# Kernel optimization log

Measured on AMD Instinct MI355X. Metric: run time of the kernel, lower is better.

## Reference

```python
import jax, jax.numpy as jnp
import numpy as np

EPS = 1e-5

def _layernorm(x, gamma, beta):
    # LayerNormalization over last axis (channels), epsilon=1e-5
    mu = jnp.mean(x, axis=-1, keepdims=True)
    var = jnp.var(x, axis=-1, keepdims=True)
    return (x - mu) * jax.lax.rsqrt(var + EPS) * gamma + beta

def setup_inputs() -> dict:
    key = jax.random.key(0)
    ks = jax.random.split(key, 6)
    B, H, W, C = 8, 64, 64, 256
    std = 0.1  # NIN init_scale
    return {
        "x": jax.random.normal(ks[0], (B, H, W, C), dtype=jnp.float32),
        "ln_gamma": jnp.ones((C,), dtype=jnp.float32),
        "ln_beta": jnp.zeros((C,), dtype=jnp.float32),
        "wq": jax.random.normal(ks[1], (C, C), dtype=jnp.float32) * std,
        "bq": jnp.zeros((C,), dtype=jnp.float32),
        "wk": jax.random.normal(ks[2], (C, C), dtype=jnp.float32) * std,
        "bk": jnp.zeros((C,), dtype=jnp.float32),
        "wv": jax.random.normal(ks[3], (C, C), dtype=jnp.float32) * std,
        "bv": jnp.zeros((C,), dtype=jnp.float32),
        "wo": jax.random.normal(ks[4], (C, C), dtype=jnp.float32) * std,
        "bo": jnp.zeros((C,), dtype=jnp.float32),
    }

def reference(x, ln_gamma, ln_beta, wq, bq, wk, bk, wv, bv, wo, bo):
    B, H, W, C = x.shape
    h = _layernorm(x, ln_gamma, ln_beta)
    # 1x1 convs == per-pixel channel matmuls
    q = jnp.einsum('bhwc,cd->bhwd', h, wq) + bq
    k = jnp.einsum('bhwc,cd->bhwd', h, wk) + bk
    v = jnp.einsum('bhwc,cd->bhwd', h, wv) + bv
    scale = jnp.float32(C) ** -0.5
    # dense spatial attention over all H*W tokens
    w = jnp.einsum('bhwc,bijc->bhwij', q, k) * scale  # [B,H,W,H,W]
    w = jax.nn.softmax(w.reshape(B, H, W, H * W), axis=-1).reshape(B, H, W, H, W)
    h = jnp.einsum('bhwij,bijc->bhwc', w, v)
    h = jnp.einsum('bhwc,cd->bhwd', h, wo) + bo
    return x + h
```

## Files before the change

### kernel.cpp

```cpp
#include <hip/hip_runtime.h>
#include <stdint.h>

#define NB    8
#define NTOK  4096
#define TOK   32768
#define CDIM  256
#define BQ    128
#define BK    64
#define NT    (NTOK / BK)

#define KPITCH 264
#define VPITCH 68
#define KTILE_SH (BK * KPITCH)
#define VTILE_SH (CDIM * VPITCH)
#define KCH   33
#define VCH   34
#define TOTCH (KCH + VCH)

typedef __attribute__((ext_vector_type(8))) short bf16x8;
typedef __attribute__((ext_vector_type(4))) float f32x4;

#define SSCALE 0.09016844f

static __device__ __forceinline__ unsigned short f2bf(float f) {
    union { float f; unsigned u; } v; v.f = f;
    unsigned r = v.u + 0x7fffu + ((v.u >> 16) & 1u);
    return (unsigned short)(r >> 16);
}

static __device__ __forceinline__ void dma16(const unsigned short* g, unsigned short* l) {
    __builtin_amdgcn_global_load_lds(
        (const __attribute__((address_space(1))) unsigned int*)g,
        (__attribute__((address_space(3))) unsigned int*)l,
        16, 0, 0);
}

__global__ __launch_bounds__(256) void prep_kernel(
        const float* __restrict__ x,
        const float* __restrict__ gamma,
        const float* __restrict__ beta,
        const float* __restrict__ w0, const float* __restrict__ w1,
        const float* __restrict__ w2, const float* __restrict__ w3,
        unsigned short* __restrict__ h_bf,
        unsigned short* __restrict__ wt) {
    int bx = blockIdx.x;
    if (bx >= TOK / 4) {
        int id = bx - TOK / 4;
        int m = id >> 8, dd = id & 255;
        const float* src = (m == 0) ? w0 : (m == 1) ? w1 : (m == 2) ? w2 : w3;
        wt[m * (CDIM * CDIM) + dd * CDIM + threadIdx.x] = f2bf(src[threadIdx.x * CDIM + dd]);
        return;
    }
    int w = threadIdx.x >> 6;
    int lane = threadIdx.x & 63;
    int token = bx * 4 + w;
    const float4 xv = ((const float4*)(x + (size_t)token * CDIM))[lane];
    float s = xv.x + xv.y + xv.z + xv.w;
    #pragma unroll
    for (int off = 1; off < 64; off <<= 1) s += __shfl_xor(s, off, 64);
    float mean = s * (1.0f / 256.0f);
    float d0 = xv.x - mean, d1 = xv.y - mean, d2 = xv.z - mean, d3 = xv.w - mean;
    float ss = d0 * d0 + d1 * d1 + d2 * d2 + d3 * d3;
    #pragma unroll
    for (int off = 1; off < 64; off <<= 1) ss += __shfl_xor(ss, off, 64);
    float rstd = rsqrtf(ss * (1.0f / 256.0f) + 1e-5f);
    float4 g = ((const float4*)gamma)[lane];
    float4 b = ((const float4*)beta)[lane];
    ushort4 o;
    o.x = f2bf(d0 * rstd * g.x + b.x);
    o.y = f2bf(d1 * rstd * g.y + b.y);
    o.z = f2bf(d2 * rstd * g.z + b.z);
    o.w = f2bf(d3 * rstd * g.w + b.w);
    ((ushort4*)(h_bf + (size_t)token * CDIM))[lane] = o;
}

__global__ __launch_bounds__(128) void qkv_kernel(
        const unsigned short* __restrict__ h_bf,
        const unsigned short* __restrict__ wts,
        const float* __restrict__ bq,
        const float* __restrict__ bk,
        const float* __restrict__ bv,
        unsigned short* __restrict__ q_bf,
        unsigned short* __restrict__ k2,
        unsigned short* __restrict__ vt2) {
    __shared__ unsigned short VT[64][VPITCH];
    int tid = threadIdx.x;
    int w = tid >> 6, lane = tid & 63, quad = lane >> 4, l16 = lane & 15;
    int blk = blockIdx.x;
    int gy = blockIdx.y;
    int nt0 = gy * 4;
    int tok_base = blk * 64 + w * 32;

    bf16x8 afr[2][8];
    #pragma unroll
    for (int s = 0; s < 2; ++s)
        #pragma unroll
        for (int kk = 0; kk < 8; ++kk)
            afr[s][kk] = *(const bf16x8*)(h_bf + (size_t)(tok_base + s * 16 + l16) * CDIM + kk * 32 + quad * 8);

    {
        const unsigned short* wq_t = wts;
        #pragma unroll
        for (int ntl = 0; ntl < 4; ++ntl) {
            int nt = nt0 + ntl;
            f32x4 acc0 = {0.f, 0.f, 0.f, 0.f};
            f32x4 acc1 = {0.f, 0.f, 0.f, 0.f};
            #pragma unroll
            for (int kk = 0; kk < 8; ++kk) {
                bf16x8 bfr = *(const bf16x8*)(wq_t + (size_t)(nt * 16 + l16) * CDIM + kk * 32 + quad * 8);
                acc0 = __builtin_amdgcn_mfma_f32_16x16x32_bf16(afr[0][kk], bfr, acc0, 0, 0, 0);
                acc1 = __builtin_amdgcn_mfma_f32_16x16x32_bf16(afr[1][kk], bfr, acc1, 0, 0, 0);
            }
            int d = nt * 16 + l16;
            float bb = bq[d];
            #pragma unroll
            for (int r = 0; r < 4; ++r) {
                q_bf[(size_t)(tok_base + quad * 4 + r) * CDIM + d]      = f2bf((acc0[r] + bb) * SSCALE);
                q_bf[(size_t)(tok_base + 16 + quad * 4 + r) * CDIM + d] = f2bf((acc1[r] + bb) * SSCALE);
            }
        }
    }
    {
        const unsigned short* wk_t = wts + CDIM * CDIM;
        unsigned short* kdst = k2 + (size_t)blk * KTILE_SH;
        int row0 = w * 32 + quad * 4;
        #pragma unroll
        for (int ntl = 0; ntl < 4; ++ntl) {
            int nt = nt0 + ntl;
            f32x4 acc0 = {0.f, 0.f, 0.f, 0.f};
            f32x4 acc1 = {0.f, 0.f, 0.f, 0.f};
            #pragma unroll
            for (int kk = 0; kk < 8; ++kk) {
                bf16x8 bfr = *(const bf16x8*)(wk_t + (size_t)(nt * 16 + l16) * CDIM + kk * 32 + quad * 8);
                acc0 = __builtin_amdgcn_mfma_f32_16x16x32_bf16(afr[0][kk], bfr, acc0, 0, 0, 0);
                acc1 = __builtin_amdgcn_mfma_f32_16x16x32_bf16(afr[1][kk], bfr, acc1, 0, 0, 0);
            }
            int d = nt * 16 + l16;
            float bb = bk[d];
            #pragma unroll
            for (int r = 0; r < 4; ++r) {
                kdst[(size_t)(row0 + r) * KPITCH + d]      = f2bf(acc0[r] + bb);
                kdst[(size_t)(row0 + 16 + r) * KPITCH + d] = f2bf(acc1[r] + bb);
            }
        }
    }
    {
        const unsigned short* wv_t = wts + 2 * CDIM * CDIM;
        int col0 = w * 32 + quad * 4;
        #pragma unroll
        for (int ntl = 0; ntl < 4; ++ntl) {
            int nt = nt0 + ntl;
            f32x4 acc0 = {0.f, 0.f, 0.f, 0.f};
            f32x4 acc1 = {0.f, 0.f, 0.f, 0.f};
            #pragma unroll
            for (int kk = 0; kk < 8; ++kk) {
                bf16x8 bfr = *(const bf16x8*)(wv_t + (size_t)(nt * 16 + l16) * CDIM + kk * 32 + quad * 8);
                acc0 = __builtin_amdgcn_mfma_f32_16x16x32_bf16(afr[0][kk], bfr, acc0, 0, 0, 0);
                acc1 = __builtin_amdgcn_mfma_f32_16x16x32_bf16(afr[1][kk], bfr, acc1, 0, 0, 0);
            }
            int d = nt * 16 + l16;
            float bb = bv[d];
            int dl = ntl * 16 + l16;
            #pragma unroll
            for (int r = 0; r < 4; ++r) {
                VT[dl][col0 + r]      = f2bf(acc0[r] + bb);
                VT[dl][col0 + 16 + r] = f2bf(acc1[r] + bb);
            }
        }
    }
    __syncthreads();
    const uint4* src = (const uint4*)(&VT[0][0]);
    uint4* dst = (uint4*)(vt2 + (size_t)blk * VTILE_SH + (size_t)gy * 64 * VPITCH);
    #pragma unroll
    for (int i = 0; i < 4; ++i)
        dst[i * 128 + tid] = src[i * 128 + tid];
    if (tid < 32) dst[512 + tid] = src[512 + tid];
}

#define DMA_TILE(KS, VS, ktn)                                                        \
    {                                                                                \
        const unsigned short* gk = k2 + (size_t)(b * NT + (ktn)) * KTILE_SH;         \
        const unsigned short* gv = vt2 + (size_t)(b * NT + (ktn)) * VTILE_SH;        \
        for (int c = w; c < TOTCH; c += 8) {                                         \
            if (c < KCH) dma16(gk + c * 512 + lane * 8, &KS[0][0] + c * 512);        \
            else dma16(gv + (c - KCH) * 512 + lane * 8, &VS[0][0] + (c - KCH) * 512);\
        }                                                                            \
    }

#define COMPUTE_TILE(KS, VS)                                                         \
    {                                                                                \
        f32x4 sfr[2][2];                                                             \
        _Pragma("unroll")                                                            \
        for (int nt = 0; nt < 2; ++nt) {                                             \
            f32x4 a0 = {0.f, 0.f, 0.f, 0.f};                                         \
            f32x4 a1 = {0.f, 0.f, 0.f, 0.f};                                         \
            _Pragma("unroll")                                                        \
            for (int kk = 0; kk < 8; ++kk) {                                         \
                bf16x8 kb = *(const bf16x8*)(&KS[kh * 32 + nt * 16 + l16][kk * 32 + quad * 8]); \
                a0 = __builtin_amdgcn_mfma_f32_16x16x32_bf16(qfr[0][kk], kb, a0, 0, 0, 0);      \
                a1 = __builtin_amdgcn_mfma_f32_16x16x32_bf16(qfr[1][kk], kb, a1, 0, 0, 0);      \
            }                                                                        \
            sfr[0][nt] = a0; sfr[1][nt] = a1;                                        \
        }                                                                            \
        _Pragma("unroll")                                                            \
        for (int s = 0; s < 2; ++s)                                                  \
            _Pragma("unroll")                                                        \
            for (int nt = 0; nt < 2; ++nt)                                           \
                _Pragma("unroll")                                                    \
                for (int r = 0; r < 4; ++r) {                                        \
                    float p = exp2f(sfr[s][nt][r]);                                  \
                    lacc[s][r] += p;                                                 \
                    Pl[wq * 32 + s * 16 + quad * 4 + r][kh * 32 + nt * 16 + l16] =   \
                        (unsigned short)(__float_as_uint(p) >> 16);                  \
                }                                                                    \
        bf16x8 pfr0 = *(const bf16x8*)(&Pl[wq * 32 + l16][kh * 32 + quad * 8]);      \
        bf16x8 pfr1 = *(const bf16x8*)(&Pl[wq * 32 + 16 + l16][kh * 32 + quad * 8]); \
        _Pragma("unroll")                                                            \
        for (int nt2 = 0; nt2 < 16; ++nt2) {                                         \
            bf16x8 vb = *(const bf16x8*)(&VS[nt2 * 16 + l16][kh * 32 + quad * 8]);   \
            O[0][nt2] = __builtin_amdgcn_mfma_f32_16x16x32_bf16(pfr0, vb, O[0][nt2], 0, 0, 0);  \
            O[1][nt2] = __builtin_amdgcn_mfma_f32_16x16x32_bf16(pfr1, vb, O[1][nt2], 0, 0, 0);  \
        }                                                                            \
    }

__global__ __launch_bounds__(512, 2) void flash_kernel(
        const unsigned short* __restrict__ q_bf,
        const unsigned short* __restrict__ k2,
        const unsigned short* __restrict__ vt2,
        unsigned short* __restrict__ attn) {
    __shared__ unsigned short Ks0[BK][KPITCH];
    __shared__ unsigned short Ks1[BK][KPITCH];
    __shared__ unsigned short Vs0[CDIM][VPITCH];
    __shared__ unsigned short Vs1[CDIM][VPITCH];
    __shared__ unsigned short Pl[BQ][VPITCH];

    int tid = threadIdx.x;
    int w = tid >> 6, lane = tid & 63, quad = lane >> 4, l16 = lane & 15;
    int kh = w >> 2;
    int wq = w & 3;
    int bid = blockIdx.x;
    int b = bid & 7;
    int qtile = bid >> 3;
    int qrow = qtile * BQ + wq * 32;
    const size_t bbase = (size_t)b * NTOK * CDIM;

    bf16x8 qfr[2][8];
    #pragma unroll
    for (int s = 0; s < 2; ++s)
        #pragma unroll
        for (int kk = 0; kk < 8; ++kk)
            qfr[s][kk] = *(const bf16x8*)(q_bf + bbase + (size_t)(qrow + s * 16 + l16) * CDIM + kk * 32 + quad * 8);

    f32x4 O[2][16];
    #pragma unroll
    for (int s = 0; s < 2; ++s)
        #pragma unroll
        for (int i = 0; i < 16; ++i) O[s][i] = (f32x4){0.f, 0.f, 0.f, 0.f};
    float lacc[2][4] = {{0.f, 0.f, 0.f, 0.f}, {0.f, 0.f, 0.f, 0.f}};

    DMA_TILE(Ks0, Vs0, 0);
    __syncthreads();

    for (int kt2 = 0; kt2 < NT; kt2 += 2) {
        DMA_TILE(Ks1, Vs1, kt2 + 1);
        COMPUTE_TILE(Ks0, Vs0);
        __syncthreads();
        if (kt2 + 2 < NT) DMA_TILE(Ks0, Vs0, kt2 + 2);
        COMPUTE_TILE(Ks1, Vs1);
        __syncthreads();
    }

    float* sO = (wq == 0) ? (float*)&Ks0[0][0] : (wq == 1) ? (float*)&Ks1[0][0]
              : (wq == 2) ? (float*)&Vs0[0][0] : (float*)&Vs1[0][0];
    float* sL = (float*)&Pl[0][0] + wq * 512;

    if (kh == 1) {
        #pragma unroll
        for (int s = 0; s < 2; ++s) {
            #pragma unroll
            for (int nt2 = 0; nt2 < 16; ++nt2)
                #pragma unroll
                for (int r = 0; r < 4; ++r)
                    sO[((s * 16 + nt2) * 4 + r) * 64 + lane] = O[s][nt2][r];
            #pragma unroll
            for (int r = 0; r < 4; ++r)
                sL[(s * 4 + r) * 64 + lane] = lacc[s][r];
        }
    }
    __syncthreads();
    if (kh == 0) {
        float linv[2][4];
        #pragma unroll
        for (int s = 0; s < 2; ++s)
            #pragma unroll
            for (int r = 0; r < 4; ++r) {
                float ls = lacc[s][r] + sL[(s * 4 + r) * 64 + lane];
                #pragma unroll
                for (int off = 1; off < 16; off <<= 1)
                    ls += __shfl_xor(ls, off, 64);
                linv[s][r] = 1.0f / ls;
            }
        #pragma unroll
        for (int s = 0; s < 2; ++s)
            #pragma unroll
            for (int nt2 = 0; nt2 < 16; ++nt2) {
                int d = nt2 * 16 + l16;
                #pragma unroll
                for (int r = 0; r < 4; ++r) {
                    float val = (O[s][nt2][r] + sO[((s * 16 + nt2) * 4 + r) * 64 + lane]) * linv[s][r];
                    attn[bbase + (size_t)(qrow + s * 16 + quad * 4 + r) * CDIM + d] = f2bf(val);
                }
            }
    }
}

__global__ __launch_bounds__(128) void oproj_kernel(
        const unsigned short* __restrict__ attn,
        const unsigned short* __restrict__ wo_t,
        const float* __restrict__ bo,
        const float* __restrict__ x,
        float* __restrict__ out) {
    int w = threadIdx.x >> 6, lane = threadIdx.x & 63;
    int quad = lane >> 4, l16 = lane & 15;
    int tok_base = blockIdx.x * 64 + w * 32;
    int nt0 = blockIdx.y * 8;

    bf16x8 afr[2][8];
    #pragma unroll
    for (int s = 0; s < 2; ++s)
        #pragma unroll
        for (int kk = 0; kk < 8; ++kk)
            afr[s][kk] = *(const bf16x8*)(attn + (size_t)(tok_base + s * 16 + l16) * CDIM + kk * 32 + quad * 8);

    #pragma unroll
    for (int ntl = 0; ntl < 8; ++ntl) {
        int nt = nt0 + ntl;
        f32x4 acc0 = {0.f, 0.f, 0.f, 0.f};
        f32x4 acc1 = {0.f, 0.f, 0.f, 0.f};
        #pragma unroll
        for (int kk = 0; kk < 8; ++kk) {
            bf16x8 bfr = *(const bf16x8*)(wo_t + (size_t)(nt * 16 + l16) * CDIM + kk * 32 + quad * 8);
            acc0 = __builtin_amdgcn_mfma_f32_16x16x32_bf16(afr[0][kk], bfr, acc0, 0, 0, 0);
            acc1 = __builtin_amdgcn_mfma_f32_16x16x32_bf16(afr[1][kk], bfr, acc1, 0, 0, 0);
        }
        int d = nt * 16 + l16;
        float bb = bo[d];
        #pragma unroll
        for (int r = 0; r < 4; ++r) {
            size_t idx0 = (size_t)(tok_base + quad * 4 + r) * CDIM + d;
            size_t idx1 = (size_t)(tok_base + 16 + quad * 4 + r) * CDIM + d;
            out[idx0] = x[idx0] + acc0[r] + bb;
            out[idx1] = x[idx1] + acc1[r] + bb;
        }
    }
}

extern "C" void kernel_launch(void* const* d_in, const int* in_sizes, int n_in,
                              void* d_out, int out_size, void* d_ws, size_t ws_size,
                              hipStream_t stream) {
    const float* x     = (const float*)d_in[0];
    const float* gamma = (const float*)d_in[1];
    const float* beta  = (const float*)d_in[2];
    const float* wq    = (const float*)d_in[3];
    const float* bq    = (const float*)d_in[4];
    const float* wk    = (const float*)d_in[5];
    const float* bk    = (const float*)d_in[6];
    const float* wv    = (const float*)d_in[7];
    const float* bv    = (const float*)d_in[8];
    const float* wo    = (const float*)d_in[9];
    const float* bo    = (const float*)d_in[10];
    float* out = (float*)d_out;

    char* ws = (char*)d_ws;
    unsigned short* h_bf = (unsigned short*)(ws);
    unsigned short* q_bf = (unsigned short*)(ws + 16777216);
    unsigned short* k2   = (unsigned short*)(ws + 33554432);
    unsigned short* vt2  = (unsigned short*)(ws + 50855936);
    unsigned short* wt   = (unsigned short*)(ws + 68681728);
    unsigned short* attn = h_bf;

    prep_kernel<<<TOK / 4 + 1024, 256, 0, stream>>>(x, gamma, beta, wq, wk, wv, wo, h_bf, wt);
    qkv_kernel<<<dim3(TOK / 64, 4), 128, 0, stream>>>(h_bf, wt, bq, bk, bv, q_bf, k2, vt2);
    flash_kernel<<<(NTOK / BQ) * NB, 512, 0, stream>>>(q_bf, k2, vt2, attn);
    oproj_kernel<<<dim3(TOK / 64, 2), 128, 0, stream>>>(attn, wt + 3 * (CDIM * CDIM), bo, x, out);
}
```

Baseline: 362.3 us.

## Split attention KV range across blocks and merge partials in separate combine kernel

```diff
diff --git a/kernel.cpp b/kernel.cpp
--- a/kernel.cpp
+++ b/kernel.cpp
@@ -5,17 +5,20 @@
 #define NTOK  4096
 #define TOK   32768
 #define CDIM  256
-#define BQ    128
-#define BK    64
-#define NT    (NTOK / BK)
-
-#define KPITCH 264
-#define VPITCH 68
-#define KTILE_SH (BK * KPITCH)
-#define VTILE_SH (CDIM * VPITCH)
-#define KCH   33
-#define VCH   34
-#define TOTCH (KCH + VCH)
+
+#define BQ2   128
+#define BK2   32
+#define NTB   128
+#define NT2   64
+
+#define KP2   272
+#define VP2   32
+#define PLP   36
+#define KTILE2_SH (BK2 * KP2)
+#define VTILE2_SH (CDIM * VP2)
+#define KCH2  17
+#define VCH2  16
+#define TOTCH2 (KCH2 + VCH2)
 
 typedef __attribute__((ext_vector_type(8))) short bf16x8;
 typedef __attribute__((ext_vector_type(4))) float f32x4;
@@ -83,7 +86,7 @@
         unsigned short* __restrict__ q_bf,
         unsigned short* __restrict__ k2,
         unsigned short* __restrict__ vt2) {
-    __shared__ unsigned short VT[64][VPITCH];
+    __shared__ unsigned short VT[64][72];
     int tid = threadIdx.x;
     int w = tid >> 6, lane = tid & 63, quad = lane >> 4, l16 = lane & 15;
     int blk = blockIdx.x;
@@ -122,8 +125,7 @@
     }
     {
         const unsigned short* wk_t = wts + CDIM * CDIM;
-        unsigned short* kdst = k2 + (size_t)blk * KTILE_SH;
-        int row0 = w * 32 + quad * 4;
+        unsigned short* kdst = k2 + (size_t)(blk * 2 + w) * KTILE2_SH;
         #pragma unroll
         for (int ntl = 0; ntl < 4; ++ntl) {
             int nt = nt0 + ntl;
@@ -139,8 +141,8 @@
             float bb = bk[d];
             #pragma unroll
             for (int r = 0; r < 4; ++r) {
-                kdst[(size_t)(row0 + r) * KPITCH + d]      = f2bf(acc0[r] + bb);
-                kdst[(size_t)(row0 + 16 + r) * KPITCH + d] = f2bf(acc1[r] + bb);
+                kdst[(size_t)(quad * 4 + r) * KP2 + d]      = f2bf(acc0[r] + bb);
+                kdst[(size_t)(quad * 4 + 16 + r) * KP2 + d] = f2bf(acc1[r] + bb);
             }
         }
     }
@@ -169,87 +171,102 @@
         }
     }
     __syncthreads();
-    const uint4* src = (const uint4*)(&VT[0][0]);
-    uint4* dst = (uint4*)(vt2 + (size_t)blk * VTILE_SH + (size_t)gy * 64 * VPITCH);
-    #pragma unroll
-    for (int i = 0; i < 4; ++i)
-        dst[i * 128 + tid] = src[i * 128 + tid];
-    if (tid < 32) dst[512 + tid] = src[512 + tid];
-}
-
-#define DMA_TILE(KS, VS, ktn)                                                        \
+    #pragma unroll
+    for (int j = 0; j < 4; ++j) {
+        int idx = j * 128 + tid;
+        int half = idx >> 8;
+        int rem = idx & 255;
+        int rr = rem >> 2;
+        int c4 = rem & 3;
+        const uint4* src = (const uint4*)(&VT[rr][half * 32 + c4 * 8]);
+        uint4* dst = (uint4*)(vt2 + (size_t)(blk * 2 + half) * VTILE2_SH
+                                   + (size_t)(gy * 64 + rr) * VP2 + c4 * 8);
+        *dst = *src;
+    }
+}
+
+#define DMA2(KS, VS, tl)                                                             \
     {                                                                                \
-        const unsigned short* gk = k2 + (size_t)(b * NT + (ktn)) * KTILE_SH;         \
-        const unsigned short* gv = vt2 + (size_t)(b * NT + (ktn)) * VTILE_SH;        \
-        for (int c = w; c < TOTCH; c += 8) {                                         \
-            if (c < KCH) dma16(gk + c * 512 + lane * 8, &KS[0][0] + c * 512);        \
-            else dma16(gv + (c - KCH) * 512 + lane * 8, &VS[0][0] + (c - KCH) * 512);\
+        const unsigned short* gk = k2 + (size_t)(tg0 + (tl)) * KTILE2_SH;            \
+        const unsigned short* gv = vt2 + (size_t)(tg0 + (tl)) * VTILE2_SH;           \
+        _Pragma("unroll")                                                            \
+        for (int i = 0; i < 9; ++i) {                                                \
+            int c = w + i * 4;                                                       \
+            if (c < TOTCH2) {                                                        \
+                if (c < KCH2) dma16(gk + c * 512 + lane * 8, &KS[0][0] + c * 512);   \
+                else dma16(gv + (c - KCH2) * 512 + lane * 8, &VS[0][0] + (c - KCH2) * 512); \
+            }                                                                        \
         }                                                                            \
     }
 
-#define COMPUTE_TILE(KS, VS)                                                         \
+#define COMPUTE2(KS, VS)                                                             \
     {                                                                                \
         f32x4 sfr[2][2];                                                             \
+        __builtin_amdgcn_s_setprio(1);                                               \
         _Pragma("unroll")                                                            \
         for (int nt = 0; nt < 2; ++nt) {                                             \
             f32x4 a0 = {0.f, 0.f, 0.f, 0.f};                                         \
             f32x4 a1 = {0.f, 0.f, 0.f, 0.f};                                         \
             _Pragma("unroll")                                                        \
             for (int kk = 0; kk < 8; ++kk) {                                         \
-                bf16x8 kb = *(const bf16x8*)(&KS[kh * 32 + nt * 16 + l16][kk * 32 + quad * 8]); \
-                a0 = __builtin_amdgcn_mfma_f32_16x16x32_bf16(qfr[0][kk], kb, a0, 0, 0, 0);      \
-                a1 = __builtin_amdgcn_mfma_f32_16x16x32_bf16(qfr[1][kk], kb, a1, 0, 0, 0);      \
+                bf16x8 kb = *(const bf16x8*)(&KS[nt * 16 + l16][kk * 32 + quad * 8]); \
+                a0 = __builtin_amdgcn_mfma_f32_16x16x32_bf16(qfr[0][kk], kb, a0, 0, 0, 0); \
+                a1 = __builtin_amdgcn_mfma_f32_16x16x32_bf16(qfr[1][kk], kb, a1, 0, 0, 0); \
             }                                                                        \
             sfr[0][nt] = a0; sfr[1][nt] = a1;                                        \
         }                                                                            \
+        __builtin_amdgcn_s_setprio(0);                                               \
         _Pragma("unroll")                                                            \
         for (int s = 0; s < 2; ++s)                                                  \
             _Pragma("unroll")                                                        \
             for (int nt = 0; nt < 2; ++nt)                                           \
                 _Pragma("unroll")                                                    \
                 for (int r = 0; r < 4; ++r) {                                        \
-                    float p = exp2f(sfr[s][nt][r]);                                  \
+                    float p = __builtin_amdgcn_exp2f(sfr[s][nt][r]);                 \
                     lacc[s][r] += p;                                                 \
-                    Pl[wq * 32 + s * 16 + quad * 4 + r][kh * 32 + nt * 16 + l16] =   \
-                        (unsigned short)(__float_as_uint(p) >> 16);                  \
+                    Pl[w * 32 + s * 16 + quad * 4 + r][nt * 16 + l16] = f2bf(p);     \
                 }                                                                    \
-        bf16x8 pfr0 = *(const bf16x8*)(&Pl[wq * 32 + l16][kh * 32 + quad * 8]);      \
-        bf16x8 pfr1 = *(const bf16x8*)(&Pl[wq * 32 + 16 + l16][kh * 32 + quad * 8]); \
+        bf16x8 pfr0 = *(const bf16x8*)(&Pl[w * 32 + l16][quad * 8]);                 \
+        bf16x8 pfr1 = *(const bf16x8*)(&Pl[w * 32 + 16 + l16][quad * 8]);            \
+        __builtin_amdgcn_s_setprio(1);                                               \
         _Pragma("unroll")                                                            \
         for (int nt2 = 0; nt2 < 16; ++nt2) {                                         \
-            bf16x8 vb = *(const bf16x8*)(&VS[nt2 * 16 + l16][kh * 32 + quad * 8]);   \
-            O[0][nt2] = __builtin_amdgcn_mfma_f32_16x16x32_bf16(pfr0, vb, O[0][nt2], 0, 0, 0);  \
-            O[1][nt2] = __builtin_amdgcn_mfma_f32_16x16x32_bf16(pfr1, vb, O[1][nt2], 0, 0, 0);  \
+            bf16x8 vb = *(const bf16x8*)(&VS[nt2 * 16 + l16][quad * 8]);             \
+            O[0][nt2] = __builtin_amdgcn_mfma_f32_16x16x32_bf16(pfr0, vb, O[0][nt2], 0, 0, 0); \
+            O[1][nt2] = __builtin_amdgcn_mfma_f32_16x16x32_bf16(pfr1, vb, O[1][nt2], 0, 0, 0); \
         }                                                                            \
-    }
-
-__global__ __launch_bounds__(512, 2) void flash_kernel(
+        __builtin_amdgcn_s_setprio(0);                                               \
+    }
+
+__global__ __launch_bounds__(256, 2) void flash_kernel(
         const unsigned short* __restrict__ q_bf,
         const unsigned short* __restrict__ k2,
         const unsigned short* __restrict__ vt2,
-        unsigned short* __restrict__ attn) {
-    __shared__ unsigned short Ks0[BK][KPITCH];
-    __shared__ unsigned short Ks1[BK][KPITCH];
-    __shared__ unsigned short Vs0[CDIM][VPITCH];
-    __shared__ unsigned short Vs1[CDIM][VPITCH];
-    __shared__ unsigned short Pl[BQ][VPITCH];
+        unsigned short* __restrict__ attn1,
+        float* __restrict__ attn0,
+        float* __restrict__ lws) {
+    __shared__ unsigned short Ks0[BK2][KP2];
+    __shared__ unsigned short Ks1[BK2][KP2];
+    __shared__ unsigned short Vs0[CDIM][VP2];
+    __shared__ unsigned short Vs1[CDIM][VP2];
+    __shared__ unsigned short Pl[BQ2][PLP];
 
     int tid = threadIdx.x;
     int w = tid >> 6, lane = tid & 63, quad = lane >> 4, l16 = lane & 15;
-    int kh = w >> 2;
-    int wq = w & 3;
     int bid = blockIdx.x;
     int b = bid & 7;
-    int qtile = bid >> 3;
-    int qrow = qtile * BQ + wq * 32;
-    const size_t bbase = (size_t)b * NTOK * CDIM;
+    int qtile = (bid >> 3) & 31;
+    int kh2 = bid >> 8;
+    int qrow = qtile * BQ2 + w * 32;
+    int rowb = b * NTOK + qrow;
+    int tg0 = b * NTB + kh2 * NT2;
 
     bf16x8 qfr[2][8];
     #pragma unroll
     for (int s = 0; s < 2; ++s)
         #pragma unroll
         for (int kk = 0; kk < 8; ++kk)
-            qfr[s][kk] = *(const bf16x8*)(q_bf + bbase + (size_t)(qrow + s * 16 + l16) * CDIM + kk * 32 + quad * 8);
+            qfr[s][kk] = *(const bf16x8*)(q_bf + (size_t)(rowb + s * 16 + l16) * CDIM + kk * 32 + quad * 8);
 
     f32x4 O[2][16];
     #pragma unroll
@@ -258,60 +275,83 @@
         for (int i = 0; i < 16; ++i) O[s][i] = (f32x4){0.f, 0.f, 0.f, 0.f};
     float lacc[2][4] = {{0.f, 0.f, 0.f, 0.f}, {0.f, 0.f, 0.f, 0.f}};
 
-    DMA_TILE(Ks0, Vs0, 0);
+    DMA2(Ks0, Vs0, 0);
     __syncthreads();
 
-    for (int kt2 = 0; kt2 < NT; kt2 += 2) {
-        DMA_TILE(Ks1, Vs1, kt2 + 1);
-        COMPUTE_TILE(Ks0, Vs0);
+    for (int kt2 = 0; kt2 < NT2; kt2 += 2) {
+        DMA2(Ks1, Vs1, kt2 + 1);
+        COMPUTE2(Ks0, Vs0);
         __syncthreads();
-        if (kt2 + 2 < NT) DMA_TILE(Ks0, Vs0, kt2 + 2);
-        COMPUTE_TILE(Ks1, Vs1);
+        if (kt2 + 2 < NT2) DMA2(Ks0, Vs0, kt2 + 2);
+        COMPUTE2(Ks1, Vs1);
         __syncthreads();
     }
 
-    float* sO = (wq == 0) ? (float*)&Ks0[0][0] : (wq == 1) ? (float*)&Ks1[0][0]
-              : (wq == 2) ? (float*)&Vs0[0][0] : (float*)&Vs1[0][0];
-    float* sL = (float*)&Pl[0][0] + wq * 512;
-
-    if (kh == 1) {
-        #pragma unroll
-        for (int s = 0; s < 2; ++s) {
+    float lred[2][4];
+    #pragma unroll
+    for (int s = 0; s < 2; ++s)
+        #pragma unroll
+        for (int r = 0; r < 4; ++r) {
+            float ls = lacc[s][r];
+            #pragma unroll
+            for (int off = 1; off < 16; off <<= 1) ls += __shfl_xor(ls, off, 64);
+            lred[s][r] = ls;
+        }
+    if (l16 == 0) {
+        #pragma unroll
+        for (int s = 0; s < 2; ++s)
+            #pragma unroll
+            for (int r = 0; r < 4; ++r)
+                lws[kh2 * TOK + rowb + s * 16 + quad * 4 + r] = lred[s][r];
+    }
+    if (kh2 == 0) {
+        #pragma unroll
+        for (int s = 0; s < 2; ++s)
             #pragma unroll
             for (int nt2 = 0; nt2 < 16; ++nt2)
                 #pragma unroll
                 for (int r = 0; r < 4; ++r)
-                    sO[((s * 16 + nt2) * 4 + r) * 64 + lane] = O[s][nt2][r];
-            #pragma unroll
-            for (int r = 0; r < 4; ++r)
-                sL[(s * 4 + r) * 64 + lane] = lacc[s][r];
-        }
-    }
-    __syncthreads();
-    if (kh == 0) {
-        float linv[2][4];
+                    attn0[(size_t)(rowb + s * 16 + quad * 4 + r) * CDIM + nt2 * 16 + l16] = O[s][nt2][r];
+    } else {
         #pragma unroll
         for (int s = 0; s < 2; ++s)
             #pragma unroll
-            for (int r = 0; r < 4; ++r) {
-                float ls = lacc[s][r] + sL[(s * 4 + r) * 64 + lane];
+            for (int nt2 = 0; nt2 < 16; ++nt2)
                 #pragma unroll
-                for (int off = 1; off < 16; off <<= 1)
-                    ls += __shfl_xor(ls, off, 64);
-                linv[s][r] = 1.0f / ls;
-            }
-        #pragma unroll
-        for (int s = 0; s < 2; ++s)
-            #pragma unroll
-            for (int nt2 = 0; nt2 < 16; ++nt2) {
-                int d = nt2 * 16 + l16;
-                #pragma unroll
-                for (int r = 0; r < 4; ++r) {
-                    float val = (O[s][nt2][r] + sO[((s * 16 + nt2) * 4 + r) * 64 + lane]) * linv[s][r];
-                    attn[bbase + (size_t)(qrow + s * 16 + quad * 4 + r) * CDIM + d] = f2bf(val);
-                }
-            }
-    }
+                for (int r = 0; r < 4; ++r)
+                    attn1[(size_t)(rowb + s * 16 + quad * 4 + r) * CDIM + nt2 * 16 + l16] = f2bf(O[s][nt2][r]);
+    }
+}
+
+__global__ __launch_bounds__(256) void combine_kernel(
+        const float* __restrict__ p0,
+        unsigned short* __restrict__ p1,
+        const float* __restrict__ lws) {
+    int t = blockIdx.x * 256 + threadIdx.x;
+    int row = t >> 5;
+    int c8 = (t & 31) * 8;
+    float inv = 1.0f / (lws[row] + lws[TOK + row]);
+    const float4* a = (const float4*)(p0 + (size_t)row * CDIM + c8);
+    float4 x0 = a[0], x1 = a[1];
+    uint4 bv = *(const uint4*)(p1 + (size_t)row * CDIM + c8);
+    float f0 = __uint_as_float((bv.x & 0xffffu) << 16);
+    float f1 = __uint_as_float(bv.x & 0xffff0000u);
+    float f2 = __uint_as_float((bv.y & 0xffffu) << 16);
+    float f3 = __uint_as_float(bv.y & 0xffff0000u);
+    float f4 = __uint_as_float((bv.z & 0xffffu) << 16);
+    float f5 = __uint_as_float(bv.z & 0xffff0000u);
+    float f6 = __uint_as_float((bv.w & 0xffffu) << 16);
+    float f7 = __uint_as_float(bv.w & 0xffff0000u);
+    float v0 = (x0.x + f0) * inv, v1 = (x0.y + f1) * inv;
+    float v2 = (x0.z + f2) * inv, v3 = (x0.w + f3) * inv;
+    float v4 = (x1.x + f4) * inv, v5 = (x1.y + f5) * inv;
+    float v6 = (x1.z + f6) * inv, v7 = (x1.w + f7) * inv;
+    uint4 o;
+    o.x = (unsigned)f2bf(v0) | ((unsigned)f2bf(v1) << 16);
+    o.y = (unsigned)f2bf(v2) | ((unsigned)f2bf(v3) << 16);
+    o.z = (unsigned)f2bf(v4) | ((unsigned)f2bf(v5) << 16);
+    o.w = (unsigned)f2bf(v6) | ((unsigned)f2bf(v7) << 16);
+    *(uint4*)(p1 + (size_t)row * CDIM + c8) = o;
 }
 
 __global__ __launch_bounds__(128) void oproj_kernel(
@@ -375,12 +415,14 @@
     unsigned short* h_bf = (unsigned short*)(ws);
     unsigned short* q_bf = (unsigned short*)(ws + 16777216);
     unsigned short* k2   = (unsigned short*)(ws + 33554432);
-    unsigned short* vt2  = (unsigned short*)(ws + 50855936);
-    unsigned short* wt   = (unsigned short*)(ws + 68681728);
+    unsigned short* vt2  = (unsigned short*)(ws + 51380224);
+    unsigned short* wt   = (unsigned short*)(ws + 68157440);
+    float* lws           = (float*)(ws + 68681728);
     unsigned short* attn = h_bf;
 
     prep_kernel<<<TOK / 4 + 1024, 256, 0, stream>>>(x, gamma, beta, wq, wk, wv, wo, h_bf, wt);
     qkv_kernel<<<dim3(TOK / 64, 4), 128, 0, stream>>>(h_bf, wt, bq, bk, bv, q_bf, k2, vt2);
-    flash_kernel<<<(NTOK / BQ) * NB, 512, 0, stream>>>(q_bf, k2, vt2, attn);
+    flash_kernel<<<512, 256, 0, stream>>>(q_bf, k2, vt2, attn, out, lws);
+    combine_kernel<<<TOK * 32 / 256, 256, 0, stream>>>(out, attn, lws);
     oproj_kernel<<<dim3(TOK / 64, 2), 128, 0, stream>>>(attn, wt + 3 * (CDIM * CDIM), bo, x, out);
 }
```

New measurement: 410.4 us. 1.13x slower.

## Swizzle K/V tiles instead of padding, use vmcnt-based pipelining and setprio

Applied to the files above, without the earlier changes.

```diff
diff --git a/kernel.cpp b/kernel.cpp
--- a/kernel.cpp
+++ b/kernel.cpp
@@ -9,13 +9,9 @@
 #define BK    64
 #define NT    (NTOK / BK)
 
-#define KPITCH 264
-#define VPITCH 68
-#define KTILE_SH (BK * KPITCH)
-#define VTILE_SH (CDIM * VPITCH)
-#define KCH   33
-#define VCH   34
-#define TOTCH (KCH + VCH)
+#define KTILE_SH (BK * CDIM)
+#define VTILE_SH (CDIM * BK)
+#define PLP   72
 
 typedef __attribute__((ext_vector_type(8))) short bf16x8;
 typedef __attribute__((ext_vector_type(4))) float f32x4;
@@ -83,7 +79,7 @@
         unsigned short* __restrict__ q_bf,
         unsigned short* __restrict__ k2,
         unsigned short* __restrict__ vt2) {
-    __shared__ unsigned short VT[64][VPITCH];
+    __shared__ unsigned short VT[64][PLP];
     int tid = threadIdx.x;
     int w = tid >> 6, lane = tid & 63, quad = lane >> 4, l16 = lane & 15;
     int blk = blockIdx.x;
@@ -139,8 +135,10 @@
             float bb = bk[d];
             #pragma unroll
             for (int r = 0; r < 4; ++r) {
-                kdst[(size_t)(row0 + r) * KPITCH + d]      = f2bf(acc0[r] + bb);
-                kdst[(size_t)(row0 + 16 + r) * KPITCH + d] = f2bf(acc1[r] + bb);
+                int k0 = row0 + r;
+                int ds = d ^ ((k0 & 7) << 3);
+                kdst[(size_t)k0 * 256 + ds]        = f2bf(acc0[r] + bb);
+                kdst[(size_t)(k0 + 16) * 256 + ds] = f2bf(acc1[r] + bb);
             }
         }
     }
@@ -169,58 +167,82 @@
         }
     }
     __syncthreads();
-    const uint4* src = (const uint4*)(&VT[0][0]);
-    uint4* dst = (uint4*)(vt2 + (size_t)blk * VTILE_SH + (size_t)gy * 64 * VPITCH);
-    #pragma unroll
-    for (int i = 0; i < 4; ++i)
-        dst[i * 128 + tid] = src[i * 128 + tid];
-    if (tid < 32) dst[512 + tid] = src[512 + tid];
+    #pragma unroll
+    for (int j = 0; j < 4; ++j) {
+        int idx = j * 128 + tid;
+        int rr = idx >> 3;
+        int c8 = idx & 7;
+        const uint4* src = (const uint4*)(&VT[rr][c8 * 8]);
+        int dsh = (gy * 64 + rr) * 64 + ((c8 * 8) ^ ((rr & 7) << 3));
+        *(uint4*)(vt2 + (size_t)blk * VTILE_SH + dsh) = *src;
+    }
 }
 
 #define DMA_TILE(KS, VS, ktn)                                                        \
     {                                                                                \
         const unsigned short* gk = k2 + (size_t)(b * NT + (ktn)) * KTILE_SH;         \
         const unsigned short* gv = vt2 + (size_t)(b * NT + (ktn)) * VTILE_SH;        \
-        for (int c = w; c < TOTCH; c += 8) {                                         \
-            if (c < KCH) dma16(gk + c * 512 + lane * 8, &KS[0][0] + c * 512);        \
-            else dma16(gv + (c - KCH) * 512 + lane * 8, &VS[0][0] + (c - KCH) * 512);\
+        _Pragma("unroll")                                                            \
+        for (int i = 0; i < 8; ++i) {                                                \
+            int c = w * 8 + i;                                                       \
+            if (c < 32) dma16(gk + c * 512 + lane * 8, &KS[0][0] + c * 512);         \
+            else dma16(gv + (c - 32) * 512 + lane * 8, &VS[0][0] + (c - 32) * 512);  \
         }                                                                            \
     }
+
+#define WAITV(N)                                             \
+    asm volatile("s_waitcnt vmcnt(" #N ")" ::: "memory");    \
+    __builtin_amdgcn_sched_barrier(0);                       \
+    __builtin_amdgcn_s_barrier();                            \
+    __builtin_amdgcn_sched_barrier(0);
+
+#define BARRIER()                                            \
+    __builtin_amdgcn_sched_barrier(0);                       \
+    __builtin_amdgcn_s_barrier();                            \
+    __builtin_amdgcn_sched_barrier(0);
 
 #define COMPUTE_TILE(KS, VS)                                                         \
     {                                                                                \
         f32x4 sfr[2][2];                                                             \
+        __builtin_amdgcn_s_setprio(1);                                               \
         _Pragma("unroll")                                                            \
         for (int nt = 0; nt < 2; ++nt) {                                             \
             f32x4 a0 = {0.f, 0.f, 0.f, 0.f};                                         \
             f32x4 a1 = {0.f, 0.f, 0.f, 0.f};                                         \
             _Pragma("unroll")                                                        \
             for (int kk = 0; kk < 8; ++kk) {                                         \
-                bf16x8 kb = *(const bf16x8*)(&KS[kh * 32 + nt * 16 + l16][kk * 32 + quad * 8]); \
+                bf16x8 kb = *(const bf16x8*)(&KS[0][0]                               \
+                    + (size_t)(kh * 32 + nt * 16 + l16) * 256                        \
+                    + ((kk * 32 + quad * 8) ^ swz));                                 \
                 a0 = __builtin_amdgcn_mfma_f32_16x16x32_bf16(qfr[0][kk], kb, a0, 0, 0, 0);      \
                 a1 = __builtin_amdgcn_mfma_f32_16x16x32_bf16(qfr[1][kk], kb, a1, 0, 0, 0);      \
             }                                                                        \
             sfr[0][nt] = a0; sfr[1][nt] = a1;                                        \
         }                                                                            \
+        __builtin_amdgcn_s_setprio(0);                                               \
         _Pragma("unroll")                                                            \
         for (int s = 0; s < 2; ++s)                                                  \
             _Pragma("unroll")                                                        \
             for (int nt = 0; nt < 2; ++nt)                                           \
                 _Pragma("unroll")                                                    \
                 for (int r = 0; r < 4; ++r) {                                        \
-                    float p = exp2f(sfr[s][nt][r]);                                  \
+                    float p = __builtin_amdgcn_exp2f(sfr[s][nt][r]);                 \
                     lacc[s][r] += p;                                                 \
                     Pl[wq * 32 + s * 16 + quad * 4 + r][kh * 32 + nt * 16 + l16] =   \
                         (unsigned short)(__float_as_uint(p) >> 16);                  \
                 }                                                                    \
         bf16x8 pfr0 = *(const bf16x8*)(&Pl[wq * 32 + l16][kh * 32 + quad * 8]);      \
         bf16x8 pfr1 = *(const bf16x8*)(&Pl[wq * 32 + 16 + l16][kh * 32 + quad * 8]); \
+        __builtin_amdgcn_s_setprio(1);                                               \
         _Pragma("unroll")                                                            \
         for (int nt2 = 0; nt2 < 16; ++nt2) {                                         \
-            bf16x8 vb = *(const bf16x8*)(&VS[nt2 * 16 + l16][kh * 32 + quad * 8]);   \
+            bf16x8 vb = *(const bf16x8*)(&VS[0][0]                                   \
+                + (size_t)(nt2 * 16 + l16) * 64                                      \
+                + ((kh * 32 + quad * 8) ^ swz));                                     \
             O[0][nt2] = __builtin_amdgcn_mfma_f32_16x16x32_bf16(pfr0, vb, O[0][nt2], 0, 0, 0);  \
             O[1][nt2] = __builtin_amdgcn_mfma_f32_16x16x32_bf16(pfr1, vb, O[1][nt2], 0, 0, 0);  \
         }                                                                            \
+        __builtin_amdgcn_s_setprio(0);                                               \
     }
 
 __global__ __launch_bounds__(512, 2) void flash_kernel(
@@ -228,16 +250,17 @@
         const unsigned short* __restrict__ k2,
         const unsigned short* __restrict__ vt2,
         unsigned short* __restrict__ attn) {
-    __shared__ unsigned short Ks0[BK][KPITCH];
-    __shared__ unsigned short Ks1[BK][KPITCH];
-    __shared__ unsigned short Vs0[CDIM][VPITCH];
-    __shared__ unsigned short Vs1[CDIM][VPITCH];
-    __shared__ unsigned short Pl[BQ][VPITCH];
+    __shared__ unsigned short Ks0[BK][256];
+    __shared__ unsigned short Ks1[BK][256];
+    __shared__ unsigned short Vs0[CDIM][64];
+    __shared__ unsigned short Vs1[CDIM][64];
+    __shared__ unsigned short Pl[BQ][PLP];
 
     int tid = threadIdx.x;
     int w = tid >> 6, lane = tid & 63, quad = lane >> 4, l16 = lane & 15;
     int kh = w >> 2;
     int wq = w & 3;
+    int swz = (l16 & 7) << 3;
     int bid = blockIdx.x;
     int b = bid & 7;
     int qtile = bid >> 3;
@@ -259,15 +282,20 @@
     float lacc[2][4] = {{0.f, 0.f, 0.f, 0.f}, {0.f, 0.f, 0.f, 0.f}};
 
     DMA_TILE(Ks0, Vs0, 0);
-    __syncthreads();
 
     for (int kt2 = 0; kt2 < NT; kt2 += 2) {
         DMA_TILE(Ks1, Vs1, kt2 + 1);
+        WAITV(8)
         COMPUTE_TILE(Ks0, Vs0);
-        __syncthreads();
-        if (kt2 + 2 < NT) DMA_TILE(Ks0, Vs0, kt2 + 2);
+        BARRIER()
+        if (kt2 + 2 < NT) {
+            DMA_TILE(Ks0, Vs0, kt2 + 2);
+            WAITV(8)
+        } else {
+            WAITV(0)
+        }
         COMPUTE_TILE(Ks1, Vs1);
-        __syncthreads();
+        BARRIER()
     }
 
     float* sO = (wq == 0) ? (float*)&Ks0[0][0] : (wq == 1) ? (float*)&Ks1[0][0]
@@ -375,8 +403,8 @@
     unsigned short* h_bf = (unsigned short*)(ws);
     unsigned short* q_bf = (unsigned short*)(ws + 16777216);
     unsigned short* k2   = (unsigned short*)(ws + 33554432);
-    unsigned short* vt2  = (unsigned short*)(ws + 50855936);
-    unsigned short* wt   = (unsigned short*)(ws + 68681728);
+    unsigned short* vt2  = (unsigned short*)(ws + 50331648);
+    unsigned short* wt   = (unsigned short*)(ws + 67108864);
     unsigned short* attn = h_bf;
 
     prep_kernel<<<TOK / 4 + 1024, 256, 0, stream>>>(x, gamma, beta, wq, wk, wv, wo, h_bf, wt);
```

New measurement: 502.0 us. 1.39x slower.

## Split flash attention block across 16 waves with 16 query rows each

Applied to the files above, without the earlier changes.

```diff
diff --git a/kernel.cpp b/kernel.cpp
--- a/kernel.cpp
+++ b/kernel.cpp
@@ -181,7 +181,7 @@
     {                                                                                \
         const unsigned short* gk = k2 + (size_t)(b * NT + (ktn)) * KTILE_SH;         \
         const unsigned short* gv = vt2 + (size_t)(b * NT + (ktn)) * VTILE_SH;        \
-        for (int c = w; c < TOTCH; c += 8) {                                         \
+        for (int c = w; c < TOTCH; c += 16) {                                        \
             if (c < KCH) dma16(gk + c * 512 + lane * 8, &KS[0][0] + c * 512);        \
             else dma16(gv + (c - KCH) * 512 + lane * 8, &VS[0][0] + (c - KCH) * 512);\
         }                                                                            \
@@ -189,41 +189,35 @@
 
 #define COMPUTE_TILE(KS, VS)                                                         \
     {                                                                                \
-        f32x4 sfr[2][2];                                                             \
+        f32x4 sfr[2];                                                                \
         _Pragma("unroll")                                                            \
         for (int nt = 0; nt < 2; ++nt) {                                             \
             f32x4 a0 = {0.f, 0.f, 0.f, 0.f};                                         \
-            f32x4 a1 = {0.f, 0.f, 0.f, 0.f};                                         \
             _Pragma("unroll")                                                        \
             for (int kk = 0; kk < 8; ++kk) {                                         \
                 bf16x8 kb = *(const bf16x8*)(&KS[kh * 32 + nt * 16 + l16][kk * 32 + quad * 8]); \
-                a0 = __builtin_amdgcn_mfma_f32_16x16x32_bf16(qfr[0][kk], kb, a0, 0, 0, 0);      \
-                a1 = __builtin_amdgcn_mfma_f32_16x16x32_bf16(qfr[1][kk], kb, a1, 0, 0, 0);      \
+                a0 = __builtin_amdgcn_mfma_f32_16x16x32_bf16(qfr[kk], kb, a0, 0, 0, 0);         \
             }                                                                        \
-            sfr[0][nt] = a0; sfr[1][nt] = a1;                                        \
+            sfr[nt] = a0;                                                            \
         }                                                                            \
         _Pragma("unroll")                                                            \
-        for (int s = 0; s < 2; ++s)                                                  \
+        for (int nt = 0; nt < 2; ++nt)                                               \
             _Pragma("unroll")                                                        \
-            for (int nt = 0; nt < 2; ++nt)                                           \
-                _Pragma("unroll")                                                    \
-                for (int r = 0; r < 4; ++r) {                                        \
-                    float p = exp2f(sfr[s][nt][r]);                                  \
-                    lacc[s][r] += p;                                                 \
-                    Pl[wq * 32 + s * 16 + quad * 4 + r][kh * 32 + nt * 16 + l16] =   \
-                        (unsigned short)(__float_as_uint(p) >> 16);                  \
-                }                                                                    \
-        bf16x8 pfr0 = *(const bf16x8*)(&Pl[wq * 32 + l16][kh * 32 + quad * 8]);      \
-        bf16x8 pfr1 = *(const bf16x8*)(&Pl[wq * 32 + 16 + l16][kh * 32 + quad * 8]); \
+            for (int r = 0; r < 4; ++r) {                                            \
+                float p = exp2f(sfr[nt][r]);                                         \
+                lacc[r] += p;                                                        \
+                Pl[wq * 16 + quad * 4 + r][kh * 32 + nt * 16 + l16] =                \
+                    (unsigned short)(__float_as_uint(p) >> 16);                      \
+            }                                                                        \
+        bf16x8 pfr = *(const bf16x8*)(&Pl[wq * 16 + l16][kh * 32 + quad * 8]);       \
         _Pragma("unroll")                                                            \
         for (int nt2 = 0; nt2 < 16; ++nt2) {                                         \
             bf16x8 vb = *(const bf16x8*)(&VS[nt2 * 16 + l16][kh * 32 + quad * 8]);   \
-            O[0][nt2] = __builtin_amdgcn_mfma_f32_16x16x32_bf16(pfr0, vb, O[0][nt2], 0, 0, 0);  \
-            O[1][nt2] = __builtin_amdgcn_mfma_f32_16x16x32_bf16(pfr1, vb, O[1][nt2], 0, 0, 0);  \
+            O[nt2] = __builtin_amdgcn_mfma_f32_16x16x32_bf16(pfr, vb, O[nt2], 0, 0, 0);         \
         }                                                                            \
     }
 
-__global__ __launch_bounds__(512, 2) void flash_kernel(
+__global__ __launch_bounds__(1024, 4) void flash_kernel(
         const unsigned short* __restrict__ q_bf,
         const unsigned short* __restrict__ k2,
         const unsigned short* __restrict__ vt2,
@@ -236,27 +230,23 @@
 
     int tid = threadIdx.x;
     int w = tid >> 6, lane = tid & 63, quad = lane >> 4, l16 = lane & 15;
-    int kh = w >> 2;
-    int wq = w & 3;
+    int kh = w >> 3;
+    int wq = w & 7;
     int bid = blockIdx.x;
     int b = bid & 7;
     int qtile = bid >> 3;
-    int qrow = qtile * BQ + wq * 32;
+    int qrow = qtile * BQ + wq * 16;
     const size_t bbase = (size_t)b * NTOK * CDIM;
 
-    bf16x8 qfr[2][8];
-    #pragma unroll
-    for (int s = 0; s < 2; ++s)
-        #pragma unroll
-        for (int kk = 0; kk < 8; ++kk)
-            qfr[s][kk] = *(const bf16x8*)(q_bf + bbase + (size_t)(qrow + s * 16 + l16) * CDIM + kk * 32 + quad * 8);
-
-    f32x4 O[2][16];
-    #pragma unroll
-    for (int s = 0; s < 2; ++s)
-        #pragma unroll
-        for (int i = 0; i < 16; ++i) O[s][i] = (f32x4){0.f, 0.f, 0.f, 0.f};
-    float lacc[2][4] = {{0.f, 0.f, 0.f, 0.f}, {0.f, 0.f, 0.f, 0.f}};
+    bf16x8 qfr[8];
+    #pragma unroll
+    for (int kk = 0; kk < 8; ++kk)
+        qfr[kk] = *(const bf16x8*)(q_bf + bbase + (size_t)(qrow + l16) * CDIM + kk * 32 + quad * 8);
+
+    f32x4 O[16];
+    #pragma unroll
+    for (int i = 0; i < 16; ++i) O[i] = (f32x4){0.f, 0.f, 0.f, 0.f};
+    float lacc[4] = {0.f, 0.f, 0.f, 0.f};
 
     DMA_TILE(Ks0, Vs0, 0);
     __syncthreads();
@@ -270,47 +260,40 @@
         __syncthreads();
     }
 
-    float* sO = (wq == 0) ? (float*)&Ks0[0][0] : (wq == 1) ? (float*)&Ks1[0][0]
-              : (wq == 2) ? (float*)&Vs0[0][0] : (float*)&Vs1[0][0];
-    float* sL = (float*)&Pl[0][0] + wq * 512;
+    float* sO = ((wq < 2) ? (float*)&Ks0[0][0] : (wq < 4) ? (float*)&Ks1[0][0]
+               : (wq < 6) ? (float*)&Vs0[0][0] : (float*)&Vs1[0][0]) + (wq & 1) * 4096;
+    float* sL = (float*)&Pl[0][0] + wq * 256;
 
     if (kh == 1) {
         #pragma unroll
-        for (int s = 0; s < 2; ++s) {
-            #pragma unroll
-            for (int nt2 = 0; nt2 < 16; ++nt2)
-                #pragma unroll
-                for (int r = 0; r < 4; ++r)
-                    sO[((s * 16 + nt2) * 4 + r) * 64 + lane] = O[s][nt2][r];
+        for (int nt2 = 0; nt2 < 16; ++nt2)
             #pragma unroll
             for (int r = 0; r < 4; ++r)
-                sL[(s * 4 + r) * 64 + lane] = lacc[s][r];
-        }
+                sO[(nt2 * 4 + r) * 64 + lane] = O[nt2][r];
+        #pragma unroll
+        for (int r = 0; r < 4; ++r)
+            sL[r * 64 + lane] = lacc[r];
     }
     __syncthreads();
     if (kh == 0) {
-        float linv[2][4];
-        #pragma unroll
-        for (int s = 0; s < 2; ++s)
+        float linv[4];
+        #pragma unroll
+        for (int r = 0; r < 4; ++r) {
+            float ls = lacc[r] + sL[r * 64 + lane];
+            #pragma unroll
+            for (int off = 1; off < 16; off <<= 1)
+                ls += __shfl_xor(ls, off, 64);
+            linv[r] = 1.0f / ls;
+        }
+        #pragma unroll
+        for (int nt2 = 0; nt2 < 16; ++nt2) {
+            int d = nt2 * 16 + l16;
             #pragma unroll
             for (int r = 0; r < 4; ++r) {
-                float ls = lacc[s][r] + sL[(s * 4 + r) * 64 + lane];
-                #pragma unroll
-                for (int off = 1; off < 16; off <<= 1)
-                    ls += __shfl_xor(ls, off, 64);
-                linv[s][r] = 1.0f / ls;
-            }
-        #pragma unroll
-        for (int s = 0; s < 2; ++s)
-            #pragma unroll
-            for (int nt2 = 0; nt2 < 16; ++nt2) {
-                int d = nt2 * 16 + l16;
-                #pragma unroll
-                for (int r = 0; r < 4; ++r) {
-                    float val = (O[s][nt2][r] + sO[((s * 16 + nt2) * 4 + r) * 64 + lane]) * linv[s][r];
-                    attn[bbase + (size_t)(qrow + s * 16 + quad * 4 + r) * CDIM + d] = f2bf(val);
-                }
-            }
+                float val = (O[nt2][r] + sO[(nt2 * 4 + r) * 64 + lane]) * linv[r];
+                attn[bbase + (size_t)(qrow + quad * 4 + r) * CDIM + d] = f2bf(val);
+            }
+        }
     }
 }
 
@@ -381,6 +364,6 @@
 
     prep_kernel<<<TOK / 4 + 1024, 256, 0, stream>>>(x, gamma, beta, wq, wk, wv, wo, h_bf, wt);
     qkv_kernel<<<dim3(TOK / 64, 4), 128, 0, stream>>>(h_bf, wt, bq, bk, bv, q_bf, k2, vt2);
-    flash_kernel<<<(NTOK / BQ) * NB, 512, 0, stream>>>(q_bf, k2, vt2, attn);
+    flash_kernel<<<(NTOK / BQ) * NB, 1024, 0, stream>>>(q_bf, k2, vt2, attn);
     oproj_kernel<<<dim3(TOK / 64, 2), 128, 0, stream>>>(attn, wt + 3 * (CDIM * CDIM), bo, x, out);
 }
```

After: 410.6 us. 13.4% more time.
